# Kernel optimization log

Measured on AMD Instinct MI355X. Metric: run time of the kernel, lower is better.

## Reference

```python
import jax, jax.numpy as jnp
import numpy as np

N, G, K = 16384, 32, 8          # cells, hvg genes (32*32 covet), n_neighs
IN_DIM, HID, OUT = 2000, 1024, 30


def setup_inputs() -> dict:
    key = jax.random.key(0)
    ks = jax.random.split(key, 8)
    return {
        "x": jax.random.normal(ks[0], (N, IN_DIM), jnp.float32),
        "coordinates": jax.random.uniform(ks[1], (N, 2), jnp.float32) * 100.0,
        "highly_variable_genes": jax.random.uniform(ks[2], (N, G), jnp.float32),
        # fc1: Linear(input_dim + 32*32, hidden); stored as [in, out]
        "W1": jax.random.normal(ks[3], (IN_DIM + G * G, HID), jnp.float32) * 0.02,
        "b1": jnp.zeros((HID,), jnp.float32),
        "W2": jax.random.normal(ks[4], (HID, OUT), jnp.float32) * 0.02,
        "b2": jnp.zeros((OUT,), jnp.float32),
    }


def _covet_sqrt(genes, coords, k):
    # brute-force kNN over spatial coordinates (squared euclidean)
    sq = jnp.sum(coords * coords, axis=1)                      # [N]
    d2 = sq[:, None] + sq[None, :] - 2.0 * (coords @ coords.T)  # [N, N]
    _, idx = jax.lax.top_k(-d2, k)                             # [N, k] nearest (incl. self)
    neigh = genes[idx]                                         # [N, k, G] irregular gather
    # COVET: center neighborhoods at the GLOBAL mean expression
    centered = neigh - jnp.mean(genes, axis=0)                 # [N, k, G]
    cov = jnp.einsum('nkg,nkh->ngh', centered, centered) / (k - 1)  # [N, G, G]
    # matrix square root of each PSD covariance via eigh
    w, V = jnp.linalg.eigh(cov)
    s = jnp.sqrt(jnp.clip(w, 0.0, None))                       # [N, G]
    return jnp.einsum('ngk,nk,nhk->ngh', V, s, V)              # V diag(s) V^T


def reference(x, coordinates, highly_variable_genes, W1, b1, W2, b2):
    # original runs covet_sqrt in numpy -> detached from autograd
    covet = jax.lax.stop_gradient(
        _covet_sqrt(highly_variable_genes, coordinates, K))
    hidden = jnp.concatenate([x, covet.reshape(-1, G * G)], axis=1)  # [N, IN+1024]
    h = jax.nn.relu(hidden @ W1 + b1)
    return h @ W2 + b2
```

## Files before the change

### kernel.cpp

```cpp
#include <hip/hip_runtime.h>
#include <hip/hip_bf16.h>
#include <math.h>

#define N_CELLS 16384
#define G_GENES 32
#define IN_DIM  2000
#define HID     1024
#define OUT_DIM 30
#define K_TOT   3024
#define K_PAD   3040
#define NT      95
#define GRID_B  128
#define NBINS   (GRID_B * GRID_B)
#define SCELL   (100.0f / (float)GRID_B)
#define CSCALE  0.37796447300922722721f

typedef unsigned short ushort_t;
typedef __attribute__((ext_vector_type(8))) short bf16x8;
typedef __attribute__((ext_vector_type(4))) short bf16x4;
typedef __attribute__((ext_vector_type(4))) float f32x4;

__device__ __forceinline__ ushort_t f2bf(float v) {
  return __builtin_bit_cast(ushort_t, __float2bfloat16(v));
}

__device__ __forceinline__ void glds16(const void* g, void* l) {
  __builtin_amdgcn_global_load_lds(
      (const __attribute__((address_space(1))) unsigned int*)g,
      (__attribute__((address_space(3))) unsigned int*)l, 16, 0, 0);
}

__global__ __launch_bounds__(256) void fused_pre(const float* __restrict__ x,
                                                 const float* __restrict__ W1,
                                                 const float* __restrict__ W2,
                                                 const float* __restrict__ genes,
                                                 const float* __restrict__ coords,
                                                 ushort_t* __restrict__ Abf,
                                                 ushort_t* __restrict__ Bh,
                                                 ushort_t* __restrict__ W2t,
                                                 double* __restrict__ part,
                                                 int* __restrict__ cnt,
                                                 int* __restrict__ binOf) {
  __shared__ float L[32][260];
  __shared__ double red[256];
  const int bid = blockIdx.x;
  const int tid = threadIdx.x;

  if (bid < 380) {
    const int cb = bid / NT, t = bid % NT;
    const int k0 = t * 32, n0 = cb * 256;
    {
      const int kl = tid >> 3;
      const int nw = tid & 7;
#pragma unroll
      for (int u = 0; u < 8; ++u) {
        const int nl = (nw + u * 8) * 4;
        float4 v = make_float4(0.f, 0.f, 0.f, 0.f);
        if (k0 + kl < K_TOT) v = *(const float4*)(W1 + (size_t)(k0 + kl) * HID + n0 + nl);
        L[kl][nl + 0] = v.x; L[kl][nl + 1] = v.y; L[kl][nl + 2] = v.z; L[kl][nl + 3] = v.w;
      }
    }
    __syncthreads();
    const size_t tileBase = ((size_t)cb * NT + t) * 8192;
    const int n = tid;
#pragma unroll
    for (int q = 0; q < 4; ++q) {
      const int cdata = q ^ ((n >> 1) & 3);
      ushort_t hi[8];
#pragma unroll
      for (int e = 0; e < 8; ++e) {
        const int kl = cdata * 8 + e;
        const float v = (k0 + kl < K_TOT) ? L[kl][n] : 0.f;
        hi[e] = f2bf(v);
      }
      *(bf16x8*)(Bh + tileBase + ((size_t)n * 4 + q) * 8) = *(const bf16x8*)hi;
    }
  } else if (bid < 384) {
    const int k = (bid - 380) * 256 + tid;
#pragma unroll
    for (int o = 0; o < 32; ++o) {
      const float v = (o < OUT_DIM) ? W2[k * OUT_DIM + o] : 0.f;
      W2t[o * HID + k] = f2bf(v);
    }
  } else if (bid < 2432) {
    const int rbase = (bid - 384) * 8;
#pragma unroll
    for (int rr = 0; rr < 8; ++rr) {
      const int row = rbase + rr;
      if (tid < 250) {
#pragma unroll
        for (int ph = 0; ph < 2; ++ph) {
          const int col = ph * 1000 + tid * 4;
          const float4 v = *(const float4*)(x + (size_t)row * IN_DIM + col);
          ushort_t o[4] = { f2bf(v.x), f2bf(v.y), f2bf(v.z), f2bf(v.w) };
          *(bf16x4*)(Abf + (size_t)row * K_PAD + col) = *(const bf16x4*)o;
        }
      } else if (tid < 252) {
        const bf16x8 z = (bf16x8){0, 0, 0, 0, 0, 0, 0, 0};
        *(bf16x8*)(Abf + (size_t)row * K_PAD + K_TOT + (tid - 250) * 8) = z;
      }
    }
  } else if (bid < 2560) {
    const int b = bid - 2432;
    const int g = tid & 31, cs = tid >> 5;
    double acc = 0.0;
#pragma unroll
    for (int it = 0; it < 16; ++it) {
      const int cell = b * 128 + cs + it * 8;
      acc += (double)genes[cell * G_GENES + g];
    }
    red[tid] = acc;
    __syncthreads();
    if (tid < 32) {
      double s = red[tid];
#pragma unroll
      for (int u = 1; u < 8; ++u) s += red[tid + u * 32];
      part[b * 32 + tid] = s;
    }
  } else {
    const int i = (bid - 2560) * 256 + tid;
    const float2 p = ((const float2*)coords)[i];
    const float inv_s = (float)GRID_B / 100.0f;
    const int bx = min(GRID_B - 1, max(0, (int)(p.x * inv_s)));
    const int by = min(GRID_B - 1, max(0, (int)(p.y * inv_s)));
    const int b = by * GRID_B + bx;
    binOf[i] = b;
    atomicAdd(&cnt[b], 1);
  }
}

__global__ __launch_bounds__(256) void scan_fin(const int* __restrict__ cnt,
                                                int* __restrict__ binStart,
                                                int* __restrict__ cursor,
                                                const double* __restrict__ part,
                                                float* __restrict__ meanv) {
  const int tid = threadIdx.x;
  if (blockIdx.x == 0) {
    __shared__ int ps[256];
    int s = 0;
    for (int i = 0; i < 64; ++i) s += cnt[tid * 64 + i];
    ps[tid] = s;
    __syncthreads();
    for (int off = 1; off < 256; off <<= 1) {
      const int add = (tid >= off) ? ps[tid - off] : 0;
      __syncthreads();
      ps[tid] += add;
      __syncthreads();
    }
    int run = ps[tid] - s;
    for (int i = 0; i < 64; ++i) {
      const int b = tid * 64 + i;
      binStart[b] = run;
      cursor[b] = run;
      run += cnt[b];
    }
    if (tid == 255) binStart[NBINS] = run;
  } else {
    if (tid < 32) {
      double s = 0.0;
      for (int b = 0; b < 128; ++b) s += part[b * 32 + tid];
      meanv[tid] = (float)(s / (double)N_CELLS);
    }
  }
}

__global__ __launch_bounds__(256) void bin_scatter(const float* __restrict__ coords,
                                                   const int* __restrict__ binOf,
                                                   int* __restrict__ cursor,
                                                   int* __restrict__ binPts,
                                                   float2* __restrict__ sxy) {
  const int i = blockIdx.x * 256 + threadIdx.x;
  const float2 p = ((const float2*)coords)[i];
  const int pos = atomicAdd(&cursor[binOf[i]], 1);
  binPts[pos] = i;
  sxy[pos] = p;
}

__global__ __launch_bounds__(128) void knn_search(const float* __restrict__ coords,
                                                  const int* __restrict__ binStart,
                                                  const int* __restrict__ binPts,
                                                  const float2* __restrict__ sxy,
                                                  int* __restrict__ nidx) {
  const int cell = blockIdx.x * 128 + threadIdx.x;
  const float qx = coords[cell * 2 + 0], qy = coords[cell * 2 + 1];
  const float sqi = __fadd_rn(__fmul_rn(qx, qx), __fmul_rn(qy, qy));
  const float inv_s = (float)GRID_B / 100.0f;
  const int bx = min(GRID_B - 1, max(0, (int)(qx * inv_s)));
  const int by = min(GRID_B - 1, max(0, (int)(qy * inv_s)));

  unsigned long long kk[8];
#pragma unroll
  for (int i = 0; i < 8; ++i) kk[i] = ~0ull;

  auto scan_seg = [&](int s, int e) {
    for (int p = s; p < e; ++p) {
      const float2 pc = sxy[p];
      const int j = binPts[p];
      const float sqj = __fadd_rn(__fmul_rn(pc.x, pc.x), __fmul_rn(pc.y, pc.y));
      const float dot = __fmaf_rn(qy, pc.y, __fmul_rn(qx, pc.x));
      const float d2  = __fsub_rn(__fadd_rn(sqi, sqj), __fmul_rn(2.0f, dot));
      unsigned int sb = __float_as_uint(d2);
      sb = (sb & 0x80000000u) ? ~sb : (sb | 0x80000000u);
      unsigned long long key = ((unsigned long long)sb << 32) | (unsigned int)j;
      if (key < kk[7]) {
#pragma unroll
        for (int q2 = 0; q2 < 8; ++q2) {
          const bool lt = key < kk[q2];
          const unsigned long long tmp = kk[q2];
          kk[q2] = lt ? key : kk[q2];
          key = lt ? tmp : key;
        }
      }
    }
  };

  bool done = false;
  for (int r = 0; r < GRID_B; ++r) {
    if (!done) {
      if (r == 0) {
        const int b = by * GRID_B + bx;
        scan_seg(binStart[b], binStart[b + 1]);
      } else {
        const int xlo = max(0, bx - r), xhi = min(GRID_B - 1, bx + r);
        if (by - r >= 0) {
          const int b0 = (by - r) * GRID_B;
          scan_seg(binStart[b0 + xlo], binStart[b0 + xhi + 1]);
        }
        if (by + r < GRID_B) {
          const int b0 = (by + r) * GRID_B;
          scan_seg(binStart[b0 + xlo], binStart[b0 + xhi + 1]);
        }
        for (int dy = -r + 1; dy <= r - 1; ++dy) {
          const int yy = by + dy;
          if (yy < 0 || yy >= GRID_B) continue;
          if (bx - r >= 0) { const int b = yy * GRID_B + bx - r; scan_seg(binStart[b], binStart[b + 1]); }
          if (bx + r < GRID_B) { const int b = yy * GRID_B + bx + r; scan_seg(binStart[b], binStart[b + 1]); }
        }
      }
      if (kk[7] != ~0ull) {
        const unsigned int sb = (unsigned int)(kk[7] >> 32);
        const float wd2 = __uint_as_float((sb & 0x80000000u) ? (sb ^ 0x80000000u) : ~sb);
        const float bnd = (float)r * SCELL;
        if (wd2 < bnd * bnd * 0.998f - 0.05f) done = true;
      }
    }
    if (!__any(!done)) break;
  }
#pragma unroll
  for (int i = 0; i < 8; ++i) nidx[cell * 8 + i] = (int)(kk[i] & 0xFFFFFFFFu);
}

__global__ __launch_bounds__(256) void gram_kernel(const float* __restrict__ genes,
                                                   const float* __restrict__ meanv,
                                                   const int* __restrict__ nidx,
                                                   float* __restrict__ GwsT) {
  const int wv = threadIdx.x >> 6, lane = threadIdx.x & 63;
  const int bidl = (blockIdx.x & 7) * 512 + (blockIdx.x >> 3);
  const int cell = bidl * 4 + wv;
  __shared__ float A[4][8][33];
#pragma unroll
  for (int q = 0; q < 4; ++q) {
    const int e = lane + (q << 6);
    const int n = e >> 5, g = e & 31;
    const int src = nidx[cell * 8 + n];
    A[wv][n][g] = (genes[src * G_GENES + g] - meanv[g]) * CSCALE;
  }
  __syncthreads();
  const int i = lane >> 3, j = lane & 7;
  float acc = 0.f;
#pragma unroll
  for (int g = 0; g < 32; ++g) acc = fmaf(A[wv][i][g], A[wv][j][g], acc);
  GwsT[(size_t)lane * N_CELLS + cell] = acc;
}

__global__ __launch_bounds__(64) void jacobi_kernel(const float* __restrict__ GwsT,
                                                    float* __restrict__ VwsT,
                                                    float* __restrict__ lamT) {
  const int cell = blockIdx.x * 64 + threadIdx.x;
  float Gm[8][8], V[8][8];
#pragma unroll
  for (int e = 0; e < 64; ++e) Gm[e >> 3][e & 7] = GwsT[(size_t)e * N_CELLS + cell];
#pragma unroll
  for (int i = 0; i < 8; ++i)
#pragma unroll
    for (int j = 0; j < 8; ++j) V[i][j] = (i == j) ? 1.0f : 0.0f;

  for (int sweep = 0; sweep < 6; ++sweep) {
#pragma unroll
    for (int p = 0; p < 7; ++p) {
#pragma unroll
      for (int q = p + 1; q < 8; ++q) {
        const float apq = Gm[p][q];
        const float app = Gm[p][p], aqq = Gm[q][q];
        float t;
        if (apq != 0.0f) {
          const float tau = (aqq - app) / (2.0f * apq);
          const float r = sqrtf(fmaf(tau, tau, 1.0f));
          t = copysignf(1.0f, tau) / (fabsf(tau) + r);
        } else {
          t = 0.0f;
        }
        const float c = 1.0f / sqrtf(fmaf(t, t, 1.0f));
        const float s = t * c;
#pragma unroll
        for (int r2 = 0; r2 < 8; ++r2) {
          const float gp = Gm[p][r2], gq = Gm[q][r2];
          Gm[p][r2] = fmaf(c, gp, -s * gq);
          Gm[q][r2] = fmaf(s, gp,  c * gq);
        }
#pragma unroll
        for (int r2 = 0; r2 < 8; ++r2) {
          const float gp = Gm[r2][p], gq = Gm[r2][q];
          Gm[r2][p] = fmaf(c, gp, -s * gq);
          Gm[r2][q] = fmaf(s, gp,  c * gq);
        }
#pragma unroll
        for (int r2 = 0; r2 < 8; ++r2) {
          const float vp = V[r2][p], vq = V[r2][q];
          V[r2][p] = fmaf(c, vp, -s * vq);
          V[r2][q] = fmaf(s, vp,  c * vq);
        }
      }
    }
  }
#pragma unroll
  for (int e = 0; e < 64; ++e) VwsT[(size_t)e * N_CELLS + cell] = V[e >> 3][e & 7];
#pragma unroll
  for (int m = 0; m < 8; ++m) lamT[(size_t)m * N_CELLS + cell] = Gm[m][m];
}

__global__ __launch_bounds__(256) void recon_kernel(const float* __restrict__ genes,
                                                    const float* __restrict__ meanv,
                                                    const int* __restrict__ nidx,
                                                    const float* __restrict__ VwsT,
                                                    const float* __restrict__ lamT,
                                                    ushort_t* __restrict__ Abf) {
  const int wv = threadIdx.x >> 6, lane = threadIdx.x & 63;
  const int cell = blockIdx.x * 4 + wv;
  __shared__ float A[4][8][33];
  __shared__ float Ws[4][8][33];
  __shared__ float Vs[4][64];
  __shared__ float lamS[4][8];
#pragma unroll
  for (int q = 0; q < 4; ++q) {
    const int e = lane + (q << 6);
    const int n = e >> 5, g = e & 31;
    const int src = nidx[cell * 8 + n];
    A[wv][n][g] = (genes[src * G_GENES + g] - meanv[g]) * CSCALE;
  }
  Vs[wv][lane] = VwsT[(size_t)lane * N_CELLS + cell];
  if (lane < 8) lamS[wv][lane] = lamT[(size_t)lane * N_CELLS + cell];
  __syncthreads();

  float maxl = 0.f;
#pragma unroll
  for (int m = 0; m < 8; ++m) maxl = fmaxf(maxl, lamS[wv][m]);
  const float thr = maxl * 1e-8f;

#pragma unroll
  for (int q = 0; q < 4; ++q) {
    const int e = lane + (q << 6);
    const int m = e >> 5, g = e & 31;
    float acc = 0.f;
#pragma unroll
    for (int i = 0; i < 8; ++i) acc = fmaf(Vs[wv][i * 8 + m], A[wv][i][g], acc);
    const float l = lamS[wv][m];
    const float scm = (l > thr) ? sqrtf(1.0f / sqrtf(l)) : 0.0f;
    Ws[wv][m][g] = acc * scm;
  }
  __syncthreads();
  ushort_t* dst = Abf + (size_t)cell * K_PAD + IN_DIM;
#pragma unroll
  for (int r = 0; r < 16; ++r) {
    const int o = (r << 6) + lane;
    const int g = o >> 5, hh = o & 31;
    float acc = 0.f;
#pragma unroll
    for (int m = 0; m < 8; ++m) acc = fmaf(Ws[wv][m][g], Ws[wv][m][hh], acc);
    dst[o] = f2bf(acc);
  }
}

__global__ __launch_bounds__(512, 4) void gemm1_kernel(const ushort_t* __restrict__ Abf,
                                                       const ushort_t* __restrict__ Bh,
                                                       const float* __restrict__ b1,
                                                       ushort_t* __restrict__ h) {
  __shared__ ushort_t As[3][4096];
  __shared__ ushort_t Bs[3][8192];

  const int tid = threadIdx.x;
  const int id  = blockIdx.x;
  const int xcd = id & 7, local = id >> 3;
  const int rb  = (xcd << 4) + (local & 15);
  const int cb  = local >> 4;
  const int row0 = rb << 7, col0 = cb << 8;

  const int lane = tid & 63, wv = tid >> 6;
  const int m_base = (wv >> 2) << 6, n_base = (wv & 3) << 6;
  const int l15 = lane & 15, l4 = lane >> 4;

  const int arow = tid >> 2, acpos = tid & 3;
  const int acdata = acpos ^ ((arow >> 1) & 3);
  const ushort_t* aptr = Abf + (size_t)(row0 + arow) * K_PAD + acdata * 8;
  const ushort_t* bptr = Bh + (size_t)cb * NT * 8192 + tid * 8;

  int aoff[4], boff[4];
#pragma unroll
  for (int i = 0; i < 4; ++i) {
    const int r = m_base + i * 16 + l15;
    aoff[i] = r * 32 + (l4 ^ ((r >> 1) & 3)) * 8;
  }
#pragma unroll
  for (int j = 0; j < 4; ++j) {
    const int r = n_base + j * 16 + l15;
    boff[j] = r * 32 + (l4 ^ ((r >> 1) & 3)) * 8;
  }

  f32x4 acc[4][4];
#pragma unroll
  for (int i = 0; i < 4; ++i)
#pragma unroll
    for (int j = 0; j < 4; ++j) acc[i][j] = (f32x4){0.f, 0.f, 0.f, 0.f};

  auto prefetch = [&](int buf) {
    glds16(aptr,        &As[buf][tid * 8]);
    glds16(bptr,        &Bs[buf][tid * 8]);
    glds16(bptr + 4096, &Bs[buf][tid * 8 + 4096]);
    aptr += 32;
    bptr += 8192;
  };
  auto compute = [&](int buf) {
    bf16x8 ah[4], bh[4];
#pragma unroll
    for (int i = 0; i < 4; ++i) ah[i] = *(const bf16x8*)(&As[buf][aoff[i]]);
#pragma unroll
    for (int j = 0; j < 4; ++j) bh[j] = *(const bf16x8*)(&Bs[buf][boff[j]]);
#pragma unroll
    for (int i = 0; i < 4; ++i)
#pragma unroll
      for (int j = 0; j < 4; ++j)
        acc[i][j] = __builtin_amdgcn_mfma_f32_16x16x32_bf16(ah[i], bh[j], acc[i][j], 0, 0, 0);
  };

  prefetch(0);
  prefetch(1);
  asm volatile("s_waitcnt vmcnt(3)" ::: "memory");
  __builtin_amdgcn_s_barrier();
  __builtin_amdgcn_sched_barrier(0);

#define STEP(BUFC, BUFP) { prefetch(BUFP); compute(BUFC); \
    asm volatile("s_waitcnt vmcnt(3)" ::: "memory"); \
    __builtin_amdgcn_s_barrier(); \
    __builtin_amdgcn_sched_barrier(0); }
  for (int tt = 0; tt < 31; ++tt) {
    STEP(0, 2)
    STEP(1, 0)
    STEP(2, 1)
  }
#undef STEP
  compute(0);
  asm volatile("s_waitcnt vmcnt(0)" ::: "memory");
  __builtin_amdgcn_s_barrier();
  __builtin_amdgcn_sched_barrier(0);
  compute(1);

  float bb[4];
#pragma unroll
  for (int j = 0; j < 4; ++j) bb[j] = b1[col0 + n_base + j * 16 + l15];
#pragma unroll
  for (int i = 0; i < 4; ++i) {
    const int rbase = row0 + m_base + i * 16 + l4 * 4;
#pragma unroll
    for (int j = 0; j < 4; ++j) {
      const int c = col0 + n_base + j * 16 + l15;
#pragma unroll
      for (int q = 0; q < 4; ++q) {
        const float v = fmaxf(acc[i][j][q] + bb[j], 0.f);
        h[(size_t)(rbase + q) * HID + c] = f2bf(v);
      }
    }
  }
}

__global__ __launch_bounds__(256) void gemm2_kernel(const ushort_t* __restrict__ h,
                                                    const ushort_t* __restrict__ W2t,
                                                    const float* __restrict__ b2,
                                                    float* __restrict__ out) {
  const int tid = threadIdx.x;
  const int lane = tid & 63, wv = tid >> 6;
  const int rowt = wv & 1, colt = wv >> 1;
  const int l15 = lane & 15, l4 = lane >> 4;
  const int row0 = blockIdx.x * 32 + rowt * 16;
  const int col  = colt * 16 + l15;

  f32x4 acc = (f32x4){0.f, 0.f, 0.f, 0.f};
  const ushort_t* ha = h + (size_t)(row0 + l15) * HID + l4 * 8;
  const ushort_t* wb = W2t + (size_t)col * HID + l4 * 8;
#pragma unroll 8
  for (int k0 = 0; k0 < HID; k0 += 32) {
    const bf16x8 av = *(const bf16x8*)(ha + k0);
    const bf16x8 bv = *(const bf16x8*)(wb + k0);
    acc = __builtin_amdgcn_mfma_f32_16x16x32_bf16(av, bv, acc, 0, 0, 0);
  }
  if (col < OUT_DIM) {
    const float bias = b2[col];
#pragma unroll
    for (int q = 0; q < 4; ++q) {
      const int r = row0 + l4 * 4 + q;
      out[(size_t)r * OUT_DIM + col] = acc[q] + bias;
    }
  }
}

extern "C" void kernel_launch(void* const* d_in, const int* in_sizes, int n_in,
                              void* d_out, int out_size, void* d_ws, size_t ws_size,
                              hipStream_t stream) {
  (void)in_sizes; (void)n_in; (void)out_size;
  const float* x      = (const float*)d_in[0];
  const float* coords = (const float*)d_in[1];
  const float* genes  = (const float*)d_in[2];
  const float* W1     = (const float*)d_in[3];
  const float* b1     = (const float*)d_in[4];
  const float* W2     = (const float*)d_in[5];
  const float* b2     = (const float*)d_in[6];
  float* out = (float*)d_out;

  char* ws = (char*)d_ws;
  size_t off = 0;
  auto alloc = [&](size_t bytes) -> void* {
    void* p = ws + off;
    off = (off + bytes + 255) & ~(size_t)255;
    return p;
  };
  ushort_t* Abf    = (ushort_t*)alloc((size_t)N_CELLS * K_PAD * 2);
  ushort_t* hbf    = (ushort_t*)alloc((size_t)N_CELLS * HID * 2);
  ushort_t* Bh     = (ushort_t*)alloc((size_t)4 * NT * 8192 * 2);
  ushort_t* W2t    = (ushort_t*)alloc((size_t)32 * HID * 2);
  float*    GwsT   = (float*)alloc((size_t)64 * N_CELLS * 4);
  float*    VwsT   = (float*)alloc((size_t)64 * N_CELLS * 4);
  float*    lamT   = (float*)alloc((size_t)8 * N_CELLS * 4);
  int*      nidx   = (int*)alloc((size_t)N_CELLS * 8 * 4);
  double*   part   = (double*)alloc((size_t)128 * 32 * 8);
  float*    meanv  = (float*)alloc(G_GENES * 4);
  int*      binCnt = (int*)alloc((size_t)NBINS * 4);
  int*      binSt  = (int*)alloc((size_t)(NBINS + 1) * 4);
  int*      cursor = (int*)alloc((size_t)NBINS * 4);
  int*      binOf  = (int*)alloc((size_t)N_CELLS * 4);
  int*      binPts = (int*)alloc((size_t)N_CELLS * 4);
  float2*   sxy    = (float2*)alloc((size_t)N_CELLS * 8);
  if (off > ws_size) return;

  hipMemsetAsync(binCnt, 0, (size_t)NBINS * 4, stream);

  hipLaunchKernelGGL(fused_pre,   dim3(2624),  dim3(256), 0, stream,
                     x, W1, W2, genes, coords, Abf, Bh, W2t, part, binCnt, binOf);
  hipLaunchKernelGGL(scan_fin,    dim3(2),     dim3(256), 0, stream, binCnt, binSt, cursor, part, meanv);
  hipLaunchKernelGGL(bin_scatter, dim3(64),    dim3(256), 0, stream, coords, binOf, cursor, binPts, sxy);
  hipLaunchKernelGGL(knn_search,  dim3(128),   dim3(128), 0, stream, coords, binSt, binPts, sxy, nidx);
  hipLaunchKernelGGL(gram_kernel, dim3(4096),  dim3(256), 0, stream, genes, meanv, nidx, GwsT);
  hipLaunchKernelGGL(jacobi_kernel, dim3(256), dim3(64),  0, stream, GwsT, VwsT, lamT);
  hipLaunchKernelGGL(recon_kernel,  dim3(4096), dim3(256), 0, stream, genes, meanv, nidx, VwsT, lamT, Abf);
  hipLaunchKernelGGL(gemm1_kernel,  dim3(512),  dim3(512), 0, stream, Abf, Bh, b1, hbf);
  hipLaunchKernelGGL(gemm2_kernel,  dim3(512),  dim3(256), 0, stream, hbf, W2t, b2, out);
}
```

Baseline: 293.1 us.

## Deepen A-tile prefetch in gemm1 and process kNN queries in bin order

The GEMM1 main loop gets a fourth A shared-memory buffer, so A tiles are prefetched three steps ahead while B stays triple-buffered. The waitcnt thresholds are adjusted to match, aiming to hide more global-load latency. Separately, kNN queries are now assigned in spatially sorted (bin) order, so neighbouring threads scan the same bins, which reduces divergence and improves cache locality. The costs are extra LDS per block, which may reduce occupancy, and a more intricate hand-tuned wait schedule.

```diff
diff --git a/kernel.cpp b/kernel.cpp
--- a/kernel.cpp
+++ b/kernel.cpp
@@ -176,13 +176,14 @@
   sxy[pos] = p;
 }
 
-__global__ __launch_bounds__(128) void knn_search(const float* __restrict__ coords,
-                                                  const int* __restrict__ binStart,
+__global__ __launch_bounds__(128) void knn_search(const int* __restrict__ binStart,
                                                   const int* __restrict__ binPts,
                                                   const float2* __restrict__ sxy,
                                                   int* __restrict__ nidx) {
-  const int cell = blockIdx.x * 128 + threadIdx.x;
-  const float qx = coords[cell * 2 + 0], qy = coords[cell * 2 + 1];
+  const int rank = blockIdx.x * 128 + threadIdx.x;
+  const int cell = binPts[rank];
+  const float2 qv = sxy[rank];
+  const float qx = qv.x, qy = qv.y;
   const float sqi = __fadd_rn(__fmul_rn(qx, qx), __fmul_rn(qy, qy));
   const float inv_s = (float)GRID_B / 100.0f;
   const int bx = min(GRID_B - 1, max(0, (int)(qx * inv_s)));
@@ -385,7 +386,7 @@
                                                        const ushort_t* __restrict__ Bh,
                                                        const float* __restrict__ b1,
                                                        ushort_t* __restrict__ h) {
-  __shared__ ushort_t As[3][4096];
+  __shared__ ushort_t As[4][4096];
   __shared__ ushort_t Bs[3][8192];
 
   const int tid = threadIdx.x;
@@ -422,19 +423,21 @@
 #pragma unroll
     for (int j = 0; j < 4; ++j) acc[i][j] = (f32x4){0.f, 0.f, 0.f, 0.f};
 
-  auto prefetch = [&](int buf) {
-    glds16(aptr,        &As[buf][tid * 8]);
+  auto gldsA = [&](int buf) {
+    glds16(aptr, &As[buf][tid * 8]);
+    aptr += 32;
+  };
+  auto gldsB = [&](int buf) {
     glds16(bptr,        &Bs[buf][tid * 8]);
     glds16(bptr + 4096, &Bs[buf][tid * 8 + 4096]);
-    aptr += 32;
     bptr += 8192;
   };
-  auto compute = [&](int buf) {
+  auto compute = [&](int ab, int bb) {
     bf16x8 ah[4], bh[4];
 #pragma unroll
-    for (int i = 0; i < 4; ++i) ah[i] = *(const bf16x8*)(&As[buf][aoff[i]]);
-#pragma unroll
-    for (int j = 0; j < 4; ++j) bh[j] = *(const bf16x8*)(&Bs[buf][boff[j]]);
+    for (int i = 0; i < 4; ++i) ah[i] = *(const bf16x8*)(&As[ab][aoff[i]]);
+#pragma unroll
+    for (int j = 0; j < 4; ++j) bh[j] = *(const bf16x8*)(&Bs[bb][boff[j]]);
 #pragma unroll
     for (int i = 0; i < 4; ++i)
 #pragma unroll
@@ -442,27 +445,31 @@
         acc[i][j] = __builtin_amdgcn_mfma_f32_16x16x32_bf16(ah[i], bh[j], acc[i][j], 0, 0, 0);
   };
 
-  prefetch(0);
-  prefetch(1);
+  gldsA(0); gldsB(0);
+  gldsA(1); gldsB(1);
+  gldsA(2);
+  asm volatile("s_waitcnt vmcnt(4)" ::: "memory");
+  __builtin_amdgcn_s_barrier();
+  __builtin_amdgcn_sched_barrier(0);
+
+  for (int t = 0; t < 92; ++t) {
+    gldsB((t + 2) % 3);
+    gldsA((t + 3) & 3);
+    compute(t & 3, t % 3);
+    asm volatile("s_waitcnt vmcnt(4)" ::: "memory");
+    __builtin_amdgcn_s_barrier();
+    __builtin_amdgcn_sched_barrier(0);
+  }
+  gldsB(94 % 3);
+  compute(92 & 3, 92 % 3);
   asm volatile("s_waitcnt vmcnt(3)" ::: "memory");
   __builtin_amdgcn_s_barrier();
   __builtin_amdgcn_sched_barrier(0);
-
-#define STEP(BUFC, BUFP) { prefetch(BUFP); compute(BUFC); \
-    asm volatile("s_waitcnt vmcnt(3)" ::: "memory"); \
-    __builtin_amdgcn_s_barrier(); \
-    __builtin_amdgcn_sched_barrier(0); }
-  for (int tt = 0; tt < 31; ++tt) {
-    STEP(0, 2)
-    STEP(1, 0)
-    STEP(2, 1)
-  }
-#undef STEP
-  compute(0);
+  compute(93 & 3, 93 % 3);
   asm volatile("s_waitcnt vmcnt(0)" ::: "memory");
   __builtin_amdgcn_s_barrier();
   __builtin_amdgcn_sched_barrier(0);
-  compute(1);
+  compute(94 & 3, 94 % 3);
 
   float bb[4];
 #pragma unroll
@@ -556,7 +563,7 @@
                      x, W1, W2, genes, coords, Abf, Bh, W2t, part, binCnt, binOf);
   hipLaunchKernelGGL(scan_fin,    dim3(2),     dim3(256), 0, stream, binCnt, binSt, cursor, part, meanv);
   hipLaunchKernelGGL(bin_scatter, dim3(64),    dim3(256), 0, stream, coords, binOf, cursor, binPts, sxy);
-  hipLaunchKernelGGL(knn_search,  dim3(128),   dim3(128), 0, stream, coords, binSt, binPts, sxy, nidx);
+  hipLaunchKernelGGL(knn_search,  dim3(128),   dim3(128), 0, stream, binSt, binPts, sxy, nidx);
   hipLaunchKernelGGL(gram_kernel, dim3(4096),  dim3(256), 0, stream, genes, meanv, nidx, GwsT);
   hipLaunchKernelGGL(jacobi_kernel, dim3(256), dim3(64),  0, stream, GwsT, VwsT, lamT);
   hipLaunchKernelGGL(recon_kernel,  dim3(4096), dim3(256), 0, stream, genes, meanv, nidx, VwsT, lamT, Abf);
```

Measured after the change: 287.3 us. 2.0% less time.

## Fuse gram, Jacobi eigensolve and reconstruction into one kernel; bin-order kNN queries

Applied to the files above, without the earlier changes.

Merges the Gram, per-cell Jacobi eigendecomposition and COVET reconstruction kernels into one kernel that keeps Gram, eigenvectors and eigenvalues for 64 cells in shared memory. This removes two launches and the global round trips of the transposed Gram, eigenvector and eigenvalue workspaces. kNN queries are now issued in spatially sorted bin order, so threads in a wavefront scan nearby bins and diverge less. The trade-off is that only 256 blocks run, and the Jacobi stage uses only one of four wavefronts per block while the others sit idle. Occupancy also drops from the large shared-memory footprint.

```diff
diff --git a/kernel.cpp b/kernel.cpp
--- a/kernel.cpp
+++ b/kernel.cpp
@@ -176,13 +176,14 @@
   sxy[pos] = p;
 }
 
-__global__ __launch_bounds__(128) void knn_search(const float* __restrict__ coords,
-                                                  const int* __restrict__ binStart,
+__global__ __launch_bounds__(128) void knn_search(const int* __restrict__ binStart,
                                                   const int* __restrict__ binPts,
                                                   const float2* __restrict__ sxy,
                                                   int* __restrict__ nidx) {
-  const int cell = blockIdx.x * 128 + threadIdx.x;
-  const float qx = coords[cell * 2 + 0], qy = coords[cell * 2 + 1];
+  const int rank = blockIdx.x * 128 + threadIdx.x;
+  const int cell = binPts[rank];
+  const float2 qv = sxy[rank];
+  const float qx = qv.x, qy = qv.y;
   const float sqi = __fadd_rn(__fmul_rn(qx, qx), __fmul_rn(qy, qy));
   const float inv_s = (float)GRID_B / 100.0f;
   const int bx = min(GRID_B - 1, max(0, (int)(qx * inv_s)));
@@ -250,134 +251,129 @@
   for (int i = 0; i < 8; ++i) nidx[cell * 8 + i] = (int)(kk[i] & 0xFFFFFFFFu);
 }
 
-__global__ __launch_bounds__(256) void gram_kernel(const float* __restrict__ genes,
+__global__ __launch_bounds__(256) void covet_fused(const float* __restrict__ genes,
                                                    const float* __restrict__ meanv,
                                                    const int* __restrict__ nidx,
-                                                   float* __restrict__ GwsT) {
-  const int wv = threadIdx.x >> 6, lane = threadIdx.x & 63;
-  const int bidl = (blockIdx.x & 7) * 512 + (blockIdx.x >> 3);
-  const int cell = bidl * 4 + wv;
-  __shared__ float A[4][8][33];
-#pragma unroll
-  for (int q = 0; q < 4; ++q) {
-    const int e = lane + (q << 6);
-    const int n = e >> 5, g = e & 31;
-    const int src = nidx[cell * 8 + n];
-    A[wv][n][g] = (genes[src * G_GENES + g] - meanv[g]) * CSCALE;
+                                                   ushort_t* __restrict__ Abf) {
+  __shared__ float As4[4][8][33];
+  __shared__ float Ws4[4][8][33];
+  __shared__ float Gt[64][65];
+  __shared__ float Vt[64][65];
+  __shared__ float lamt[8][65];
+
+  const int tid = threadIdx.x;
+  const int wv = tid >> 6, lane = tid & 63;
+  const int base = blockIdx.x * 64;
+
+  for (int cc = 0; cc < 16; ++cc) {
+    const int local = wv * 16 + cc;
+    const int cell = base + local;
+#pragma unroll
+    for (int q = 0; q < 4; ++q) {
+      const int e = lane + (q << 6);
+      const int n = e >> 5, g = e & 31;
+      const int src = nidx[cell * 8 + n];
+      As4[wv][n][g] = (genes[src * G_GENES + g] - meanv[g]) * CSCALE;
+    }
+    const int i = lane >> 3, j = lane & 7;
+    float acc = 0.f;
+#pragma unroll
+    for (int g = 0; g < 32; ++g) acc = fmaf(As4[wv][i][g], As4[wv][j][g], acc);
+    Gt[lane][local] = acc;
   }
   __syncthreads();
-  const int i = lane >> 3, j = lane & 7;
-  float acc = 0.f;
-#pragma unroll
-  for (int g = 0; g < 32; ++g) acc = fmaf(A[wv][i][g], A[wv][j][g], acc);
-  GwsT[(size_t)lane * N_CELLS + cell] = acc;
-}
-
-__global__ __launch_bounds__(64) void jacobi_kernel(const float* __restrict__ GwsT,
-                                                    float* __restrict__ VwsT,
-                                                    float* __restrict__ lamT) {
-  const int cell = blockIdx.x * 64 + threadIdx.x;
-  float Gm[8][8], V[8][8];
-#pragma unroll
-  for (int e = 0; e < 64; ++e) Gm[e >> 3][e & 7] = GwsT[(size_t)e * N_CELLS + cell];
-#pragma unroll
-  for (int i = 0; i < 8; ++i)
-#pragma unroll
-    for (int j = 0; j < 8; ++j) V[i][j] = (i == j) ? 1.0f : 0.0f;
-
-  for (int sweep = 0; sweep < 6; ++sweep) {
-#pragma unroll
-    for (int p = 0; p < 7; ++p) {
-#pragma unroll
-      for (int q = p + 1; q < 8; ++q) {
-        const float apq = Gm[p][q];
-        const float app = Gm[p][p], aqq = Gm[q][q];
-        float t;
-        if (apq != 0.0f) {
-          const float tau = (aqq - app) / (2.0f * apq);
-          const float r = sqrtf(fmaf(tau, tau, 1.0f));
-          t = copysignf(1.0f, tau) / (fabsf(tau) + r);
-        } else {
-          t = 0.0f;
+
+  if (tid < 64) {
+    const int cl = tid;
+    float Gm[8][8], V[8][8];
+#pragma unroll
+    for (int e = 0; e < 64; ++e) Gm[e >> 3][e & 7] = Gt[e][cl];
+#pragma unroll
+    for (int i = 0; i < 8; ++i)
+#pragma unroll
+      for (int j = 0; j < 8; ++j) V[i][j] = (i == j) ? 1.0f : 0.0f;
+
+    for (int sweep = 0; sweep < 6; ++sweep) {
+#pragma unroll
+      for (int p = 0; p < 7; ++p) {
+#pragma unroll
+        for (int q = p + 1; q < 8; ++q) {
+          const float apq = Gm[p][q];
+          const float app = Gm[p][p], aqq = Gm[q][q];
+          float t;
+          if (apq != 0.0f) {
+            const float tau = (aqq - app) / (2.0f * apq);
+            const float r = sqrtf(fmaf(tau, tau, 1.0f));
+            t = copysignf(1.0f, tau) / (fabsf(tau) + r);
+          } else {
+            t = 0.0f;
+          }
+          const float c = 1.0f / sqrtf(fmaf(t, t, 1.0f));
+          const float s = t * c;
+#pragma unroll
+          for (int r2 = 0; r2 < 8; ++r2) {
+            const float gp = Gm[p][r2], gq = Gm[q][r2];
+            Gm[p][r2] = fmaf(c, gp, -s * gq);
+            Gm[q][r2] = fmaf(s, gp,  c * gq);
+          }
+#pragma unroll
+          for (int r2 = 0; r2 < 8; ++r2) {
+            const float gp = Gm[r2][p], gq = Gm[r2][q];
+            Gm[r2][p] = fmaf(c, gp, -s * gq);
+            Gm[r2][q] = fmaf(s, gp,  c * gq);
+          }
+#pragma unroll
+          for (int r2 = 0; r2 < 8; ++r2) {
+            const float vp = V[r2][p], vq = V[r2][q];
+            V[r2][p] = fmaf(c, vp, -s * vq);
+            V[r2][q] = fmaf(s, vp,  c * vq);
+          }
         }
-        const float c = 1.0f / sqrtf(fmaf(t, t, 1.0f));
-        const float s = t * c;
-#pragma unroll
-        for (int r2 = 0; r2 < 8; ++r2) {
-          const float gp = Gm[p][r2], gq = Gm[q][r2];
-          Gm[p][r2] = fmaf(c, gp, -s * gq);
-          Gm[q][r2] = fmaf(s, gp,  c * gq);
-        }
-#pragma unroll
-        for (int r2 = 0; r2 < 8; ++r2) {
-          const float gp = Gm[r2][p], gq = Gm[r2][q];
-          Gm[r2][p] = fmaf(c, gp, -s * gq);
-          Gm[r2][q] = fmaf(s, gp,  c * gq);
-        }
-#pragma unroll
-        for (int r2 = 0; r2 < 8; ++r2) {
-          const float vp = V[r2][p], vq = V[r2][q];
-          V[r2][p] = fmaf(c, vp, -s * vq);
-          V[r2][q] = fmaf(s, vp,  c * vq);
-        }
-      }
-    }
-  }
-#pragma unroll
-  for (int e = 0; e < 64; ++e) VwsT[(size_t)e * N_CELLS + cell] = V[e >> 3][e & 7];
-#pragma unroll
-  for (int m = 0; m < 8; ++m) lamT[(size_t)m * N_CELLS + cell] = Gm[m][m];
-}
-
-__global__ __launch_bounds__(256) void recon_kernel(const float* __restrict__ genes,
-                                                    const float* __restrict__ meanv,
-                                                    const int* __restrict__ nidx,
-                                                    const float* __restrict__ VwsT,
-                                                    const float* __restrict__ lamT,
-                                                    ushort_t* __restrict__ Abf) {
-  const int wv = threadIdx.x >> 6, lane = threadIdx.x & 63;
-  const int cell = blockIdx.x * 4 + wv;
-  __shared__ float A[4][8][33];
-  __shared__ float Ws[4][8][33];
-  __shared__ float Vs[4][64];
-  __shared__ float lamS[4][8];
-#pragma unroll
-  for (int q = 0; q < 4; ++q) {
-    const int e = lane + (q << 6);
-    const int n = e >> 5, g = e & 31;
-    const int src = nidx[cell * 8 + n];
-    A[wv][n][g] = (genes[src * G_GENES + g] - meanv[g]) * CSCALE;
-  }
-  Vs[wv][lane] = VwsT[(size_t)lane * N_CELLS + cell];
-  if (lane < 8) lamS[wv][lane] = lamT[(size_t)lane * N_CELLS + cell];
+      }
+    }
+#pragma unroll
+    for (int e = 0; e < 64; ++e) Vt[e][cl] = V[e >> 3][e & 7];
+#pragma unroll
+    for (int m = 0; m < 8; ++m) lamt[m][cl] = Gm[m][m];
+  }
   __syncthreads();
 
-  float maxl = 0.f;
-#pragma unroll
-  for (int m = 0; m < 8; ++m) maxl = fmaxf(maxl, lamS[wv][m]);
-  const float thr = maxl * 1e-8f;
-
-#pragma unroll
-  for (int q = 0; q < 4; ++q) {
-    const int e = lane + (q << 6);
-    const int m = e >> 5, g = e & 31;
-    float acc = 0.f;
-#pragma unroll
-    for (int i = 0; i < 8; ++i) acc = fmaf(Vs[wv][i * 8 + m], A[wv][i][g], acc);
-    const float l = lamS[wv][m];
-    const float scm = (l > thr) ? sqrtf(1.0f / sqrtf(l)) : 0.0f;
-    Ws[wv][m][g] = acc * scm;
-  }
-  __syncthreads();
-  ushort_t* dst = Abf + (size_t)cell * K_PAD + IN_DIM;
-#pragma unroll
-  for (int r = 0; r < 16; ++r) {
-    const int o = (r << 6) + lane;
-    const int g = o >> 5, hh = o & 31;
-    float acc = 0.f;
-#pragma unroll
-    for (int m = 0; m < 8; ++m) acc = fmaf(Ws[wv][m][g], Ws[wv][m][hh], acc);
-    dst[o] = f2bf(acc);
+  for (int cc = 0; cc < 16; ++cc) {
+    const int local = wv * 16 + cc;
+    const int cell = base + local;
+#pragma unroll
+    for (int q = 0; q < 4; ++q) {
+      const int e = lane + (q << 6);
+      const int n = e >> 5, g = e & 31;
+      const int src = nidx[cell * 8 + n];
+      As4[wv][n][g] = (genes[src * G_GENES + g] - meanv[g]) * CSCALE;
+    }
+    float maxl = 0.f;
+#pragma unroll
+    for (int m = 0; m < 8; ++m) maxl = fmaxf(maxl, lamt[m][local]);
+    const float thr = maxl * 1e-8f;
+
+#pragma unroll
+    for (int q = 0; q < 4; ++q) {
+      const int e = lane + (q << 6);
+      const int m = e >> 5, g = e & 31;
+      float acc = 0.f;
+#pragma unroll
+      for (int i = 0; i < 8; ++i) acc = fmaf(Vt[i * 8 + m][local], As4[wv][i][g], acc);
+      const float l = lamt[m][local];
+      const float scm = (l > thr) ? sqrtf(1.0f / sqrtf(l)) : 0.0f;
+      Ws4[wv][m][g] = acc * scm;
+    }
+    ushort_t* dst = Abf + (size_t)cell * K_PAD + IN_DIM;
+#pragma unroll
+    for (int r = 0; r < 16; ++r) {
+      const int o = (r << 6) + lane;
+      const int g = o >> 5, hh = o & 31;
+      float acc = 0.f;
+#pragma unroll
+      for (int m = 0; m < 8; ++m) acc = fmaf(Ws4[wv][m][g], Ws4[wv][m][hh], acc);
+      dst[o] = f2bf(acc);
+    }
   }
 }
 
@@ -536,9 +532,6 @@
   ushort_t* hbf    = (ushort_t*)alloc((size_t)N_CELLS * HID * 2);
   ushort_t* Bh     = (ushort_t*)alloc((size_t)4 * NT * 8192 * 2);
   ushort_t* W2t    = (ushort_t*)alloc((size_t)32 * HID * 2);
-  float*    GwsT   = (float*)alloc((size_t)64 * N_CELLS * 4);
-  float*    VwsT   = (float*)alloc((size_t)64 * N_CELLS * 4);
-  float*    lamT   = (float*)alloc((size_t)8 * N_CELLS * 4);
   int*      nidx   = (int*)alloc((size_t)N_CELLS * 8 * 4);
   double*   part   = (double*)alloc((size_t)128 * 32 * 8);
   float*    meanv  = (float*)alloc(G_GENES * 4);
@@ -556,10 +549,8 @@
                      x, W1, W2, genes, coords, Abf, Bh, W2t, part, binCnt, binOf);
   hipLaunchKernelGGL(scan_fin,    dim3(2),     dim3(256), 0, stream, binCnt, binSt, cursor, part, meanv);
   hipLaunchKernelGGL(bin_scatter, dim3(64),    dim3(256), 0, stream, coords, binOf, cursor, binPts, sxy);
-  hipLaunchKernelGGL(knn_search,  dim3(128),   dim3(128), 0, stream, coords, binSt, binPts, sxy, nidx);
-  hipLaunchKernelGGL(gram_kernel, dim3(4096),  dim3(256), 0, stream, genes, meanv, nidx, GwsT);
-  hipLaunchKernelGGL(jacobi_kernel, dim3(256), dim3(64),  0, stream, GwsT, VwsT, lamT);
-  hipLaunchKernelGGL(recon_kernel,  dim3(4096), dim3(256), 0, stream, genes, meanv, nidx, VwsT, lamT, Abf);
-  hipLaunchKernelGGL(gemm1_kernel,  dim3(512),  dim3(512), 0, stream, Abf, Bh, b1, hbf);
-  hipLaunchKernelGGL(gemm2_kernel,  dim3(512),  dim3(256), 0, stream, hbf, W2t, b2, out);
-}
+  hipLaunchKernelGGL(knn_search,  dim3(128),   dim3(128), 0, stream, binSt, binPts, sxy, nidx);
+  hipLaunchKernelGGL(covet_fused, dim3(256),   dim3(256), 0, stream, genes, meanv, nidx, Abf);
+  hipLaunchKernelGGL(gemm1_kernel, dim3(512),  dim3(512), 0, stream, Abf, Bh, b1, hbf);
+  hipLaunchKernelGGL(gemm2_kernel, dim3(512),  dim3(256), 0, stream, hbf, W2t, b2, out);
+}
```

Measured after the change: 304.4 us. 1.04x slower.
